# Kernel tuning notes

Hardware: AMD Instinct MI355X
Metric: run time of the kernel (lower is better)

## Reference

```python
import jax, jax.numpy as jnp
import numpy as np
import math
from jax.ops import segment_sum

TOPK_RATIO = 0.1
CLUSTER_RATIO = 0.25
K_KNN = 10


def setup_inputs() -> dict:
    key = jax.random.key(0)
    ks = jax.random.split(key, 10)
    N, C, H, W = 8, 256, 100, 352
    sc = 0.02
    return {
        "spatial_features_2d": jax.random.normal(ks[0], (N, C, H, W), jnp.float32),
        "dis_priority": jax.random.uniform(ks[1], (N, H, W), dtype=jnp.float32),
        "score_w1": jax.random.normal(ks[2], (256, 256), jnp.float32) * sc,
        "score_b1": jnp.zeros((256,), jnp.float32),
        "score_w2": jax.random.normal(ks[3], (1, 256), jnp.float32) * sc,
        "score_b2": jnp.zeros((1,), jnp.float32),
        "cls_w": jax.random.normal(ks[4], (2, 256), jnp.float32) * sc,
        "cls_b": jnp.zeros((2,), jnp.float32),
        "reg_w": jax.random.normal(ks[5], (14, 256), jnp.float32) * sc,
        "reg_b": jnp.zeros((14,), jnp.float32),
        "record_len": jnp.array([2, 3, 1, 2], jnp.int32),
    }


def _forward(x, dis_priority, score_w1, score_b1, score_w2, score_b2,
             cls_w, cls_b, reg_w, reg_b, record_len):
    N, C, H, W = x.shape
    L = H * W
    xf = x.reshape(N, C, L)  # [N,C,L]

    # --- SortSampler: per-pixel 2-layer fc score net (1x1 convs) ---
    h = jax.nn.relu(jnp.einsum('oc,ncl->nol', score_w1, xf) + score_b1[None, :, None])
    scores = jax.nn.sigmoid(jnp.einsum('oc,ncl->nol', score_w2, h) + score_b2[None, :, None])[:, 0]  # [N,L]
    weight = scores * dis_priority.reshape(N, L)
    K = max(int(math.ceil(L * TOPK_RATIO)), 1)  # static topk token count
    sort_idx = jnp.argsort(-weight, axis=1)[:, :K]              # pos_embed [N,K]
    conf = jnp.take_along_axis(weight, sort_idx, axis=1)        # [N,K]
    feats = jnp.take_along_axis(xf, sort_idx[:, None, :], axis=2)  # [N,C,K]
    src = jnp.transpose(feats, (0, 2, 1)) * conf[:, :, None]    # [N,K,C]

    # --- cluster_dpc_knn ---
    M = max(int(math.ceil(K * CLUSTER_RATIO)), 1)
    sq = jnp.sum(src * src, axis=-1)                             # [N,K]
    dist = sq[:, :, None] + sq[:, None, :] - 2.0 * jnp.einsum('nkc,njc->nkj', src, src)
    dist = jnp.maximum(dist, 0.0)                                # [N,K,K]
    dist_nearest = -jax.lax.top_k(-dist, K_KNN)[0]               # [N,K,k] smallest
    density = jnp.exp(-jnp.mean(dist_nearest, axis=-1))          # [N,K]
    density = density + jnp.arange(K, dtype=density.dtype) * 1e-6  # deterministic tie-break
    higher = density[:, None, :] > density[:, :, None]           # [N,K,K]
    dist_max = jnp.max(dist)
    d_higher = jnp.where(higher, dist, dist_max)
    delta = jnp.min(d_higher, axis=-1)                           # [N,K]
    score = delta * density
    idx_centers = jax.lax.top_k(score, M)[1]                     # [N,M]
    # assign each token to nearest cluster center
    dist_centers = jnp.take_along_axis(dist, idx_centers[:, :, None], axis=1)  # [N,M,K]
    idx_cluster = jnp.argmin(dist_centers, axis=1)               # [N,K]
    idx_cluster = idx_cluster.at[jnp.arange(N)[:, None], idx_centers].set(
        jnp.broadcast_to(jnp.arange(M), (N, M)))

    # --- merge_tokens: weighted average per cluster ---
    flat_seg = (idx_cluster + jnp.arange(N, dtype=idx_cluster.dtype)[:, None] * M).reshape(-1)
    w = conf.reshape(-1)
    all_w = segment_sum(w, flat_seg, num_segments=N * M) + 1e-6          # [N*M]
    merged = segment_sum((src * conf[:, :, None]).reshape(N * K, C), flat_seg,
                         num_segments=N * M) / all_w[:, None]
    merged = merged.reshape(N, M, C)
    # index_points: broadcast merged cluster feature back to each token
    src_tok = jnp.take_along_axis(merged, idx_cluster[:, :, None], axis=1)  # [N,K,C]
    src_ct = jnp.transpose(src_tok, (0, 2, 1))                   # [N,C,K]

    # --- scatter tokens back into BEV grid ---
    def scat(idxs, f):  # idxs [K], f [C,K]
        return jnp.zeros((C, L), f.dtype).at[:, idxs].set(f)
    bev = jax.vmap(scat)(sort_idx, src_ct)                       # [N,C,L]
    # ego CAVs (index 0 within each record) keep the full dense feature
    offsets = jnp.concatenate([jnp.zeros((1,), jnp.int32),
                               jnp.cumsum(record_len)[:-1].astype(jnp.int32)])
    is_ego = jnp.any(jnp.arange(N)[:, None] == offsets[None, :], axis=1)  # [N]
    bev = jnp.where(is_ego[:, None, None], xf, bev).reshape(N, C, H, W)

    # --- ego heads (1x1 convs) ---
    ego = x[offsets]                                              # [B,C,H,W]
    psm_ego = jnp.einsum('oc,bchw->bohw', cls_w, ego) + cls_b[None, :, None, None]
    rm_ego = jnp.einsum('oc,bchw->bohw', reg_w, ego) + reg_b[None, :, None, None]
    return bev, psm_ego, rm_ego


def reference(spatial_features_2d, dis_priority, score_w1, score_b1, score_w2, score_b2,
              cls_w, cls_b, reg_w, reg_b, record_len):
    return _forward(spatial_features_2d, dis_priority, score_w1, score_b1, score_w2,
                    score_b2, cls_w, cls_b, reg_w, reg_b, record_len)
```

## Files before the change

kernel.cpp:

```cpp
#include <hip/hip_runtime.h>
#include <hip/hip_bf16.h>

#define CCH   256
#define LPIX  35200
#define KSEL  3520
#define MCL   880
#define NBINS 16384
#define FMAXV 3.402823466e38f

__global__ void transpose_w1(const float* __restrict__ w1, float* __restrict__ w1t) {
    int o = blockIdx.x, c = threadIdx.x;
    w1t[c * 256 + o] = w1[o * 256 + c];
}

__global__ __launch_bounds__(256) void score_kernel(
    const float* __restrict__ x, const float* __restrict__ prio,
    const float* __restrict__ w1t, const float* __restrict__ b1,
    const float* __restrict__ w2, const float* __restrict__ b2,
    float* __restrict__ weight) {
    int n = blockIdx.y;
    int l0 = blockIdx.x * 64;
    int tid = threadIdx.x;
    __shared__ float W1s[16][256];
    __shared__ float Xs[16][64];
    __shared__ float spart[64][33];
    const float* xb = x + (size_t)n * CCH * LPIX;
    int to = tid >> 3;
    int tl = tid & 7;
    float acc[8][8] = {};
    for (int c0 = 0; c0 < 256; c0 += 16) {
#pragma unroll
        for (int u = 0; u < 4; u++) {
            int id = tid + u * 256;
            int cc = id >> 6, o4 = (id & 63) << 2;
            *(float4*)&W1s[cc][o4] = *(const float4*)&w1t[(size_t)(c0 + cc) * 256 + o4];
        }
        {
            int cc = tid >> 4, l4 = (tid & 15) << 2;
            *(float4*)&Xs[cc][l4] = *(const float4*)&xb[(size_t)(c0 + cc) * LPIX + l0 + l4];
        }
        __syncthreads();
#pragma unroll
        for (int cc = 0; cc < 16; cc++) {
            float a[8], bb[8];
            *(float4*)&a[0]  = *(float4*)&W1s[cc][to * 8];
            *(float4*)&a[4]  = *(float4*)&W1s[cc][to * 8 + 4];
            *(float4*)&bb[0] = *(float4*)&Xs[cc][tl * 8];
            *(float4*)&bb[4] = *(float4*)&Xs[cc][tl * 8 + 4];
#pragma unroll
            for (int i = 0; i < 8; i++)
#pragma unroll
                for (int j = 0; j < 8; j++) acc[i][j] += a[i] * bb[j];
        }
        __syncthreads();
    }
    float w2v[8], b1v[8];
    *(float4*)&b1v[0] = *(const float4*)&b1[to * 8];
    *(float4*)&b1v[4] = *(const float4*)&b1[to * 8 + 4];
    *(float4*)&w2v[0] = *(const float4*)&w2[to * 8];
    *(float4*)&w2v[4] = *(const float4*)&w2[to * 8 + 4];
#pragma unroll
    for (int j = 0; j < 8; j++) {
        float s = 0.f;
#pragma unroll
        for (int i = 0; i < 8; i++) s += w2v[i] * fmaxf(acc[i][j] + b1v[i], 0.f);
        spart[tl * 8 + j][to] = s;
    }
    __syncthreads();
    if (tid < 64) {
        float s = 0.f;
#pragma unroll
        for (int r = 0; r < 32; r++) s += spart[tid][r];
        s += b2[0];
        float sg = 1.f / (1.f + expf(-s));
        int gl = l0 + tid;
        weight[(size_t)n * LPIX + gl] = sg * prio[(size_t)n * LPIX + gl];
    }
}

__global__ void hist_kernel(const float* __restrict__ weight, int* __restrict__ hist) {
    int n = blockIdx.y;
    int i = blockIdx.x * 256 + threadIdx.x;
    if (i >= LPIX) return;
    float w = weight[(size_t)n * LPIX + i];
    int b = (int)(w * (float)NBINS);
    b = min(max(b, 0), NBINS - 1);
    atomicAdd(&hist[(size_t)n * NBINS + b], 1);
}

__global__ __launch_bounds__(256) void thr_kernel(const int* __restrict__ hist, int* __restrict__ thrbin) {
    int n = blockIdx.x, t = threadIdx.x;
    const int CH = NBINS / 256;
    __shared__ int csum[256];
    __shared__ int bfound;
    int base = NBINS - (t + 1) * CH;
    int s = 0;
    for (int i = 0; i < CH; i++) s += hist[(size_t)n * NBINS + base + i];
    csum[t] = s;
    __syncthreads();
    if (t == 0) {
        int cum = 0, sel = 255;
        for (int u = 0; u < 256; u++) {
            cum += csum[u];
            csum[u] = cum;
            if (cum >= KSEL) { sel = u; break; }
        }
        bfound = sel;
    }
    __syncthreads();
    if (t == 0) {
        int u = bfound;
        int cumBefore = (u == 0) ? 0 : csum[u - 1];
        int base2 = NBINS - (u + 1) * CH;
        int cum = cumBefore, bsel = base2;
        for (int b = base2 + CH - 1; b >= base2; b--) {
            cum += hist[(size_t)n * NBINS + b];
            if (cum >= KSEL) { bsel = b; break; }
        }
        thrbin[n] = bsel;
    }
}

__global__ void cand_kernel(const float* __restrict__ weight, const int* __restrict__ thrbin,
                            float* __restrict__ candw, int* __restrict__ cidx, int* __restrict__ ccnt) {
    int n = blockIdx.y;
    int i = blockIdx.x * 256 + threadIdx.x;
    if (i >= LPIX) return;
    float w = weight[(size_t)n * LPIX + i];
    int b = (int)(w * (float)NBINS);
    b = min(max(b, 0), NBINS - 1);
    if (b >= thrbin[n]) {
        int p = atomicAdd(&ccnt[n], 1);
        candw[(size_t)n * LPIX + p] = w;
        cidx[(size_t)n * LPIX + p] = i;
    }
}

__global__ __launch_bounds__(256) void rank_kernel(const float* __restrict__ candw, const int* __restrict__ cidx,
                                                   const int* __restrict__ ccnt,
                                                   float* __restrict__ conf, int* __restrict__ sidx) {
    int n = blockIdx.y, i = blockIdx.x;
    int cnt = ccnt[n];
    if (i >= cnt) return;
    float wi = candw[(size_t)n * LPIX + i];
    int ii = cidx[(size_t)n * LPIX + i];
    int r = 0;
    for (int j = threadIdx.x; j < cnt; j += 256) {
        float wj = candw[(size_t)n * LPIX + j];
        int ij = cidx[(size_t)n * LPIX + j];
        if (wj > wi || (wj == wi && ij < ii)) r++;
    }
    __shared__ int red[256];
    red[threadIdx.x] = r;
    __syncthreads();
    for (int s = 128; s > 0; s >>= 1) {
        if (threadIdx.x < s) red[threadIdx.x] += red[threadIdx.x + s];
        __syncthreads();
    }
    if (threadIdx.x == 0) {
        int rank = red[0];
        if (rank < KSEL) {
            sidx[(size_t)n * KSEL + rank] = ii;
            conf[(size_t)n * KSEL + rank] = wi;
        }
    }
}

__global__ __launch_bounds__(256) void gather_src(const float* __restrict__ x, const int* __restrict__ sidx,
                                                  const float* __restrict__ conf,
                                                  float* __restrict__ src, float* __restrict__ sq, int* __restrict__ inv) {
    int n = blockIdx.y, k = blockIdx.x, c = threadIdx.x;
    int idx = sidx[(size_t)n * KSEL + k];
    float cf = conf[(size_t)n * KSEL + k];
    float v = x[((size_t)n * CCH + c) * LPIX + idx] * cf;
    src[((size_t)n * KSEL + k) * CCH + c] = v;
    __shared__ float red[256];
    red[c] = v * v;
    __syncthreads();
    for (int s = 128; s > 0; s >>= 1) {
        if (c < s) red[c] += red[c + s];
        __syncthreads();
    }
    if (c == 0) {
        sq[(size_t)n * KSEL + k] = red[0];
        inv[(size_t)n * LPIX + idx] = k;
    }
}

__global__ __launch_bounds__(256) void dist_gemm(const float* __restrict__ src, const float* __restrict__ sq,
                                                 float* __restrict__ dist, int n0) {
    int n = n0 + blockIdx.z;
    const float* S = src + (size_t)n * KSEL * CCH;
    const float* sqn = sq + (size_t)n * KSEL;
    float* D = dist + (size_t)blockIdx.z * KSEL * KSEL;
    int b = blockIdx.x;
    int iT = (int)((sqrtf(8.f * (float)b + 1.f) - 1.f) * 0.5f);
    while ((iT + 1) * (iT + 2) / 2 <= b) iT++;
    while (iT * (iT + 1) / 2 > b) iT--;
    int jT = b - iT * (iT + 1) / 2;
    int bi = iT * 128, bj = jT * 128;
    __shared__ float As[16][128], Bs[16][128];
    int tid = threadIdx.x;
    int ti = tid >> 4, to = tid & 15;
    int sr = tid >> 1;
    int sc = (tid & 1) * 8;
    int ra = min(bi + sr, KSEL - 1);
    int rb = min(bj + sr, KSEL - 1);
    float acc[8][8] = {};
    for (int c0 = 0; c0 < CCH; c0 += 16) {
        float4 a0 = *(const float4*)&S[(size_t)ra * CCH + c0 + sc];
        float4 a1 = *(const float4*)&S[(size_t)ra * CCH + c0 + sc + 4];
        float4 b0 = *(const float4*)&S[(size_t)rb * CCH + c0 + sc];
        float4 b1 = *(const float4*)&S[(size_t)rb * CCH + c0 + sc + 4];
        __syncthreads();
        As[sc + 0][sr] = a0.x; As[sc + 1][sr] = a0.y; As[sc + 2][sr] = a0.z; As[sc + 3][sr] = a0.w;
        As[sc + 4][sr] = a1.x; As[sc + 5][sr] = a1.y; As[sc + 6][sr] = a1.z; As[sc + 7][sr] = a1.w;
        Bs[sc + 0][sr] = b0.x; Bs[sc + 1][sr] = b0.y; Bs[sc + 2][sr] = b0.z; Bs[sc + 3][sr] = b0.w;
        Bs[sc + 4][sr] = b1.x; Bs[sc + 5][sr] = b1.y; Bs[sc + 6][sr] = b1.z; Bs[sc + 7][sr] = b1.w;
        __syncthreads();
#pragma unroll
        for (int cc = 0; cc < 16; cc++) {
            float a[8], bb[8];
            *(float4*)&a[0]  = *(float4*)&As[cc][ti * 8];
            *(float4*)&a[4]  = *(float4*)&As[cc][ti * 8 + 4];
            *(float4*)&bb[0] = *(float4*)&Bs[cc][to * 8];
            *(float4*)&bb[4] = *(float4*)&Bs[cc][to * 8 + 4];
#pragma unroll
            for (int i = 0; i < 8; i++)
#pragma unroll
                for (int j = 0; j < 8; j++) acc[i][j] += a[i] * bb[j];
        }
    }
    if (bi + ti * 8 < KSEL && bj + to * 8 < KSEL) {
        float sqj[8];
        *(float4*)&sqj[0] = *(const float4*)&sqn[bj + to * 8];
        *(float4*)&sqj[4] = *(const float4*)&sqn[bj + to * 8 + 4];
        float d[8][8];
#pragma unroll
        for (int i = 0; i < 8; i++) {
            float si = sqn[bi + ti * 8 + i];
#pragma unroll
            for (int j = 0; j < 8; j++) d[i][j] = fmaxf(si + sqj[j] - 2.f * acc[i][j], 0.f);
        }
#pragma unroll
        for (int i = 0; i < 8; i++) {
            int gi = bi + ti * 8 + i;
            *(float4*)&D[(size_t)gi * KSEL + bj + to * 8]     = *(float4*)&d[i][0];
            *(float4*)&D[(size_t)gi * KSEL + bj + to * 8 + 4] = *(float4*)&d[i][4];
        }
        if (iT != jT) {
#pragma unroll
            for (int j = 0; j < 8; j++) {
                int gj = bj + to * 8 + j;
                float4 t0, t1;
                t0.x = d[0][j]; t0.y = d[1][j]; t0.z = d[2][j]; t0.w = d[3][j];
                t1.x = d[4][j]; t1.y = d[5][j]; t1.z = d[6][j]; t1.w = d[7][j];
                *(float4*)&D[(size_t)gj * KSEL + bi + ti * 8]     = t0;
                *(float4*)&D[(size_t)gj * KSEL + bi + ti * 8 + 4] = t1;
            }
        }
    }
}

__global__ __launch_bounds__(256) void knn_density(const float* __restrict__ dist, float* __restrict__ density, int n0) {
    int n = n0 + blockIdx.y;
    int row = threadIdx.x >> 6;
    int lane = threadIdx.x & 63;
    int i = blockIdx.x * 4 + row;
    const float4* row4 = (const float4*)(dist + (size_t)blockIdx.y * KSEL * KSEL + (size_t)i * KSEL);
    float tt[10];
#pragma unroll
    for (int r = 0; r < 10; r++) tt[r] = FMAXV;
    for (int j4 = lane; j4 < KSEL / 4; j4 += 64) {
        float4 v4 = row4[j4];
        float vv[4] = {v4.x, v4.y, v4.z, v4.w};
#pragma unroll
        for (int q = 0; q < 4; q++) {
            float v = vv[q];
            if (v < tt[9]) {
                tt[9] = v;
#pragma unroll
                for (int r = 9; r > 0; r--) {
                    if (tt[r] < tt[r - 1]) { float tmp = tt[r - 1]; tt[r - 1] = tt[r]; tt[r] = tmp; }
                }
            }
        }
    }
    __shared__ float ls[4][64][10];
#pragma unroll
    for (int r = 0; r < 10; r++) ls[row][lane][r] = tt[r];
    __syncthreads();
    for (int s = 32; s >= 1; s >>= 1) {
        if (lane < s) {
            float out[10];
            int ia = 0, ib = 0;
#pragma unroll
            for (int r = 0; r < 10; r++) {
                float va = ls[row][lane][ia], vb = ls[row][lane + s][ib];
                if (va <= vb) { out[r] = va; ia++; } else { out[r] = vb; ib++; }
            }
#pragma unroll
            for (int r = 0; r < 10; r++) ls[row][lane][r] = out[r];
        }
        __syncthreads();
    }
    if (lane == 0) {
        float sum = 0.f;
#pragma unroll
        for (int r = 0; r < 10; r++) sum += ls[row][0][r];
        density[(size_t)n * KSEL + i] = expf(-sum * 0.1f) + (float)i * 1e-6f;
    }
}

__global__ __launch_bounds__(256) void delta_score(const float* __restrict__ dist, const float* __restrict__ density,
                                                   float* __restrict__ scoreb, int n0) {
    int n = n0 + blockIdx.y;
    int i = blockIdx.x;
    const float4* row = (const float4*)(dist + (size_t)blockIdx.y * KSEL * KSEL + (size_t)i * KSEL);
    const float* dn = density + (size_t)n * KSEL;
    const float4* dn4 = (const float4*)dn;
    float di = dn[i];
    float mn = FMAXV;
    for (int j4 = threadIdx.x; j4 < KSEL / 4; j4 += 256) {
        float4 d = dn4[j4];
        float4 v = row[j4];
        if (d.x > di) mn = fminf(mn, v.x);
        if (d.y > di) mn = fminf(mn, v.y);
        if (d.z > di) mn = fminf(mn, v.z);
        if (d.w > di) mn = fminf(mn, v.w);
    }
    __shared__ float red[256];
    red[threadIdx.x] = mn;
    __syncthreads();
    for (int s = 128; s > 0; s >>= 1) {
        if (threadIdx.x < s) red[threadIdx.x] = fminf(red[threadIdx.x], red[threadIdx.x + s]);
        __syncthreads();
    }
    if (threadIdx.x == 0) {
        float d = red[0];
        scoreb[(size_t)n * KSEL + i] = (d == FMAXV) ? FMAXV : d * di;
    }
}

__global__ __launch_bounds__(256) void center_rank(const float* __restrict__ scoreb, int* __restrict__ centers,
                                                   int* __restrict__ crank, int n0) {
    int n = n0 + blockIdx.y;
    int i = blockIdx.x;
    const float* sc = scoreb + (size_t)n * KSEL;
    float si = sc[i];
    int r = 0;
    for (int j = threadIdx.x; j < KSEL; j += 256) {
        float sj = sc[j];
        if (sj > si || (sj == si && j < i)) r++;
    }
    __shared__ int red[256];
    red[threadIdx.x] = r;
    __syncthreads();
    for (int s = 128; s > 0; s >>= 1) {
        if (threadIdx.x < s) red[threadIdx.x] += red[threadIdx.x + s];
        __syncthreads();
    }
    if (threadIdx.x == 0) {
        int rank = red[0];
        if (rank < MCL) {
            centers[(size_t)n * MCL + rank] = i;
            crank[(size_t)n * KSEL + i] = rank;
        }
    }
}

__global__ __launch_bounds__(256) void assign_kernel(const float* __restrict__ dist, const int* __restrict__ centers,
                                                     const int* __restrict__ crank, int* __restrict__ clus, int n0) {
    int n = n0 + blockIdx.y;
    const float* D = dist + (size_t)blockIdx.y * KSEL * KSEL;
    int kl = threadIdx.x & 63, mc = threadIdx.x >> 6;
    int k = blockIdx.x * 64 + kl;
    const int* ctr = centers + (size_t)n * MCL;
    float mn = FMAXV;
    int am = MCL;
    for (int m = mc * 220; m < (mc + 1) * 220; m++) {
        float v = D[(size_t)ctr[m] * KSEL + k];
        if (v < mn) { mn = v; am = m; }
    }
    __shared__ float mv[4][64];
    __shared__ int mi[4][64];
    mv[mc][kl] = mn;
    mi[mc][kl] = am;
    __syncthreads();
    if (mc == 0) {
        float best = mv[0][kl];
        int bm = mi[0][kl];
#pragma unroll
        for (int c = 1; c < 4; c++) {
            float v = mv[c][kl];
            int im = mi[c][kl];
            if (v < best || (v == best && im < bm)) { best = v; bm = im; }
        }
        int cr = crank[(size_t)n * KSEL + k];
        clus[(size_t)n * KSEL + k] = (cr >= 0) ? cr : bm;
    }
}

__global__ void merge_w(const float* __restrict__ conf, const int* __restrict__ clus, float* __restrict__ allw, int n0) {
    int n = n0 + blockIdx.y;
    int k = blockIdx.x * 256 + threadIdx.x;
    if (k >= KSEL) return;
    atomicAdd(&allw[(size_t)n * MCL + clus[(size_t)n * KSEL + k]], conf[(size_t)n * KSEL + k]);
}

__global__ void merge_feat(const float* __restrict__ src, const float* __restrict__ conf,
                           const int* __restrict__ clus, float* __restrict__ merged, int n0) {
    int n = n0 + blockIdx.y;
    int k = blockIdx.x, c = threadIdx.x;
    float v = src[((size_t)n * KSEL + k) * CCH + c] * conf[(size_t)n * KSEL + k];
    atomicAdd(&merged[((size_t)n * MCL + clus[(size_t)n * KSEL + k]) * CCH + c], v);
}

__global__ void merged_div(float* __restrict__ merged, const float* __restrict__ allw) {
    int nm = blockIdx.x, c = threadIdx.x;
    merged[(size_t)nm * CCH + c] /= (allw[nm] + 1e-6f);
}

__global__ __launch_bounds__(256) void bev_kernel(const float* __restrict__ x, const int* __restrict__ inv,
                                                  const int* __restrict__ clus, const float* __restrict__ merged,
                                                  const int* __restrict__ reclen, int B, float* __restrict__ out) {
    int n = blockIdx.y;
    int l0 = (blockIdx.x * 256 + threadIdx.x) * 4;
    if (l0 >= LPIX) return;
    bool ego = false;
    {
        int off = 0;
        for (int b = 0; b < B; b++) {
            if (n == off) { ego = true; break; }
            off += reclen[b];
        }
    }
    size_t base = (size_t)n * CCH * LPIX + l0;
    if (ego) {
        for (int c = 0; c < CCH; c++)
            *(float4*)&out[base + (size_t)c * LPIX] = *(const float4*)&x[base + (size_t)c * LPIX];
    } else {
        const float* mr0; const float* mr1; const float* mr2; const float* mr3;
        {
            int t0 = inv[(size_t)n * LPIX + l0 + 0];
            int t1 = inv[(size_t)n * LPIX + l0 + 1];
            int t2 = inv[(size_t)n * LPIX + l0 + 2];
            int t3 = inv[(size_t)n * LPIX + l0 + 3];
            mr0 = (t0 >= 0) ? merged + ((size_t)n * MCL + clus[(size_t)n * KSEL + t0]) * CCH : nullptr;
            mr1 = (t1 >= 0) ? merged + ((size_t)n * MCL + clus[(size_t)n * KSEL + t1]) * CCH : nullptr;
            mr2 = (t2 >= 0) ? merged + ((size_t)n * MCL + clus[(size_t)n * KSEL + t2]) * CCH : nullptr;
            mr3 = (t3 >= 0) ? merged + ((size_t)n * MCL + clus[(size_t)n * KSEL + t3]) * CCH : nullptr;
        }
        for (int c = 0; c < CCH; c++) {
            float4 v;
            v.x = mr0 ? mr0[c] : 0.f;
            v.y = mr1 ? mr1[c] : 0.f;
            v.z = mr2 ? mr2[c] : 0.f;
            v.w = mr3 ? mr3[c] : 0.f;
            *(float4*)&out[base + (size_t)c * LPIX] = v;
        }
    }
}

__global__ __launch_bounds__(256) void heads_kernel(const float* __restrict__ x,
                                                    const float* __restrict__ clsw, const float* __restrict__ clsb,
                                                    const float* __restrict__ regw, const float* __restrict__ regb,
                                                    const int* __restrict__ reclen,
                                                    float* __restrict__ psm, float* __restrict__ rm) {
    int b = blockIdx.y;
    int l0 = (blockIdx.x * 256 + threadIdx.x) * 4;
    __shared__ float ws[16][256];
    __shared__ float bs[16];
    for (int i = threadIdx.x; i < 16 * 256; i += 256) {
        int o = i >> 8, c = i & 255;
        ws[o][c] = (o < 2) ? clsw[o * 256 + c] : regw[(o - 2) * 256 + c];
    }
    if (threadIdx.x < 16) bs[threadIdx.x] = (threadIdx.x < 2) ? clsb[threadIdx.x] : regb[threadIdx.x - 2];
    __syncthreads();
    if (l0 >= LPIX) return;
    int off = 0;
    for (int u = 0; u < b; u++) off += reclen[u];
    const float* xb = x + (size_t)off * CCH * LPIX;
    float acc[16][4] = {};
    for (int c = 0; c < CCH; c++) {
        float4 v = *(const float4*)&xb[(size_t)c * LPIX + l0];
#pragma unroll
        for (int o = 0; o < 16; o++) {
            float w = ws[o][c];
            acc[o][0] += w * v.x; acc[o][1] += w * v.y; acc[o][2] += w * v.z; acc[o][3] += w * v.w;
        }
    }
#pragma unroll
    for (int o = 0; o < 2; o++) {
        float4 r;
        r.x = acc[o][0] + bs[o]; r.y = acc[o][1] + bs[o]; r.z = acc[o][2] + bs[o]; r.w = acc[o][3] + bs[o];
        *(float4*)&psm[((size_t)b * 2 + o) * LPIX + l0] = r;
    }
#pragma unroll
    for (int o = 0; o < 14; o++) {
        float4 r;
        float bb = bs[o + 2];
        r.x = acc[o + 2][0] + bb; r.y = acc[o + 2][1] + bb; r.z = acc[o + 2][2] + bb; r.w = acc[o + 2][3] + bb;
        *(float4*)&rm[((size_t)b * 14 + o) * LPIX + l0] = r;
    }
}

extern "C" void kernel_launch(void* const* d_in, const int* in_sizes, int n_in,
                              void* d_out, int out_size, void* d_ws, size_t ws_size,
                              hipStream_t stream) {
    const float* x    = (const float*)d_in[0];
    const float* prio = (const float*)d_in[1];
    const float* w1   = (const float*)d_in[2];
    const float* b1   = (const float*)d_in[3];
    const float* w2   = (const float*)d_in[4];
    const float* b2   = (const float*)d_in[5];
    const float* clsw = (const float*)d_in[6];
    const float* clsb = (const float*)d_in[7];
    const float* regw = (const float*)d_in[8];
    const float* regb = (const float*)d_in[9];
    const int* reclen = (const int*)d_in[10];
    int N = in_sizes[0] / (CCH * LPIX);
    int B = in_sizes[10];
    float* out = (float*)d_out;

    char* p = (char*)d_ws;
    size_t off = 0;
    auto alloc = [&](size_t bytes) -> void* {
        void* r = p + off;
        off += (bytes + 255) & ~(size_t)255;
        return r;
    };
    float* w1t     = (float*)alloc(256 * 256 * 4);
    float* weight  = (float*)alloc((size_t)N * LPIX * 4);
    int*   hist    = (int*)alloc((size_t)N * NBINS * 4);
    int*   thrbin  = (int*)alloc((size_t)N * 4);
    int*   ccnt    = (int*)alloc((size_t)N * 4);
    float* candw   = (float*)alloc((size_t)N * LPIX * 4);
    int*   cidx    = (int*)alloc((size_t)N * LPIX * 4);
    int*   sidx    = (int*)alloc((size_t)N * KSEL * 4);
    float* conf    = (float*)alloc((size_t)N * KSEL * 4);
    float* src     = (float*)alloc((size_t)N * KSEL * CCH * 4);
    float* sq      = (float*)alloc((size_t)N * KSEL * 4);
    int*   inv     = (int*)alloc((size_t)N * LPIX * 4);
    float* density = (float*)alloc((size_t)N * KSEL * 4);
    float* scoreb  = (float*)alloc((size_t)N * KSEL * 4);
    int*   centers = (int*)alloc((size_t)N * MCL * 4);
    int*   crank   = (int*)alloc((size_t)N * KSEL * 4);
    int*   clus    = (int*)alloc((size_t)N * KSEL * 4);
    float* allw    = (float*)alloc((size_t)N * MCL * 4);
    float* merged  = (float*)alloc((size_t)N * MCL * CCH * 4);
    const size_t distB = (size_t)KSEL * KSEL * 4;
    size_t rem = (ws_size > off) ? (ws_size - off) : 0;
    int nd = (int)(rem / distB);
    if (nd < 1) nd = 1;
    if (nd > N) nd = N;
    float* dist = (float*)alloc(distB * nd);

    hipMemsetAsync(hist, 0, (size_t)N * NBINS * 4, stream);
    hipMemsetAsync(ccnt, 0, (size_t)N * 4, stream);
    hipMemsetAsync(inv, 0xFF, (size_t)N * LPIX * 4, stream);
    hipMemsetAsync(crank, 0xFF, (size_t)N * KSEL * 4, stream);
    hipMemsetAsync(allw, 0, (size_t)N * MCL * 4, stream);
    hipMemsetAsync(merged, 0, (size_t)N * MCL * CCH * 4, stream);

    transpose_w1<<<256, 256, 0, stream>>>(w1, w1t);
    score_kernel<<<dim3(LPIX / 64, N), 256, 0, stream>>>(x, prio, w1t, b1, w2, b2, weight);
    hist_kernel<<<dim3((LPIX + 255) / 256, N), 256, 0, stream>>>(weight, hist);
    thr_kernel<<<N, 256, 0, stream>>>(hist, thrbin);
    cand_kernel<<<dim3((LPIX + 255) / 256, N), 256, 0, stream>>>(weight, thrbin, candw, cidx, ccnt);
    rank_kernel<<<dim3(8192, N), 256, 0, stream>>>(candw, cidx, ccnt, conf, sidx);
    gather_src<<<dim3(KSEL, N), 256, 0, stream>>>(x, sidx, conf, src, sq, inv);

    const int TI = (KSEL + 127) / 128;
    const int NT = TI * (TI + 1) / 2;
    for (int g = 0; g < N; g += nd) {
        int nb = (N - g < nd) ? (N - g) : nd;
        dist_gemm<<<dim3(NT, 1, nb), 256, 0, stream>>>(src, sq, dist, g);
        knn_density<<<dim3(KSEL / 4, nb), 256, 0, stream>>>(dist, density, g);
        delta_score<<<dim3(KSEL, nb), 256, 0, stream>>>(dist, density, scoreb, g);
        center_rank<<<dim3(KSEL, nb), 256, 0, stream>>>(scoreb, centers, crank, g);
        assign_kernel<<<dim3(KSEL / 64, nb), 256, 0, stream>>>(dist, centers, crank, clus, g);
        merge_w<<<dim3((KSEL + 255) / 256, nb), 256, 0, stream>>>(conf, clus, allw, g);
        merge_feat<<<dim3(KSEL, nb), 256, 0, stream>>>(src, conf, clus, merged, g);
    }
    merged_div<<<N * MCL, 256, 0, stream>>>(merged, allw);
    bev_kernel<<<dim3((LPIX / 4 + 255) / 256, N), 256, 0, stream>>>(x, inv, clus, merged, reclen, B, out);

    float* psm = out + (size_t)N * CCH * LPIX;
    float* rm  = psm + (size_t)B * 2 * LPIX;
    heads_kernel<<<dim3((LPIX / 4 + 255) / 256, B), 256, 0, stream>>>(x, clsw, clsb, regw, regb, reclen, psm, rm);
}
```

Baseline: 1.575 ms.

## Use split-bf16 MFMA for score net and pairwise distance GEMMs

Replaces the FP32 scalar-FMA GEMMs in the score network and the pairwise distance computation with MFMA bf16 matrix instructions. Each operand is split three ways (hi/mid/lo bf16), and six cross-product MFMAs per tile recover near-FP32 accuracy. The distance kernel drops the triangular-tile scheme with mirrored writes and computes the full square grid directly. This trades 6x more matrix ops, extra split storage and bandwidth, and the lost symmetry savings for much higher MFMA throughput.

```diff
diff --git a/kernel.cpp b/kernel.cpp
--- a/kernel.cpp
+++ b/kernel.cpp
@@ -8,73 +8,111 @@
 #define NBINS 16384
 #define FMAXV 3.402823466e38f
 
-__global__ void transpose_w1(const float* __restrict__ w1, float* __restrict__ w1t) {
-    int o = blockIdx.x, c = threadIdx.x;
-    w1t[c * 256 + o] = w1[o * 256 + c];
-}
-
-__global__ __launch_bounds__(256) void score_kernel(
+typedef __bf16 bf16x8 __attribute__((ext_vector_type(8)));
+typedef float  f32x4  __attribute__((ext_vector_type(4)));
+typedef unsigned short ushort_t;
+
+__device__ __forceinline__ void split3(float v, __bf16* h, __bf16* m, __bf16* l) {
+    __bf16 a = (__bf16)v;
+    float r = v - (float)a;
+    __bf16 b = (__bf16)r;
+    float r2 = r - (float)b;
+    *h = a; *m = b; *l = (__bf16)r2;
+}
+
+#define MFMA6(ACC, AH, AM, AL, BH, BM, BL)                                   \
+    ACC = __builtin_amdgcn_mfma_f32_16x16x32_bf16(AH, BH, ACC, 0, 0, 0);     \
+    ACC = __builtin_amdgcn_mfma_f32_16x16x32_bf16(AH, BM, ACC, 0, 0, 0);     \
+    ACC = __builtin_amdgcn_mfma_f32_16x16x32_bf16(AM, BH, ACC, 0, 0, 0);     \
+    ACC = __builtin_amdgcn_mfma_f32_16x16x32_bf16(AH, BL, ACC, 0, 0, 0);     \
+    ACC = __builtin_amdgcn_mfma_f32_16x16x32_bf16(AM, BM, ACC, 0, 0, 0);     \
+    ACC = __builtin_amdgcn_mfma_f32_16x16x32_bf16(AL, BH, ACC, 0, 0, 0);
+
+__global__ void split_w1(const float* __restrict__ w1, __bf16* __restrict__ h,
+                         __bf16* __restrict__ m, __bf16* __restrict__ l) {
+    int i = blockIdx.x * 256 + threadIdx.x;
+    split3(w1[i], &h[i], &m[i], &l[i]);
+}
+
+__global__ __launch_bounds__(256) void score_mfma(
     const float* __restrict__ x, const float* __restrict__ prio,
-    const float* __restrict__ w1t, const float* __restrict__ b1,
-    const float* __restrict__ w2, const float* __restrict__ b2,
+    const __bf16* __restrict__ w1h, const __bf16* __restrict__ w1m, const __bf16* __restrict__ w1l,
+    const float* __restrict__ b1, const float* __restrict__ w2, const float* __restrict__ b2,
     float* __restrict__ weight) {
     int n = blockIdx.y;
     int l0 = blockIdx.x * 64;
-    int tid = threadIdx.x;
-    __shared__ float W1s[16][256];
-    __shared__ float Xs[16][64];
-    __shared__ float spart[64][33];
+    int tid = threadIdx.x, w = tid >> 6, lane = tid & 63;
+    int lrow = lane & 15, kg = lane >> 4;
+    __shared__ __align__(16) __bf16 Xs[3][64][40];
+    __shared__ float spart[64][17];
     const float* xb = x + (size_t)n * CCH * LPIX;
-    int to = tid >> 3;
-    int tl = tid & 7;
-    float acc[8][8] = {};
-    for (int c0 = 0; c0 < 256; c0 += 16) {
-#pragma unroll
-        for (int u = 0; u < 4; u++) {
-            int id = tid + u * 256;
-            int cc = id >> 6, o4 = (id & 63) << 2;
-            *(float4*)&W1s[cc][o4] = *(const float4*)&w1t[(size_t)(c0 + cc) * 256 + o4];
-        }
-        {
-            int cc = tid >> 4, l4 = (tid & 15) << 2;
-            *(float4*)&Xs[cc][l4] = *(const float4*)&xb[(size_t)(c0 + cc) * LPIX + l0 + l4];
-        }
-        __syncthreads();
-#pragma unroll
-        for (int cc = 0; cc < 16; cc++) {
-            float a[8], bb[8];
-            *(float4*)&a[0]  = *(float4*)&W1s[cc][to * 8];
-            *(float4*)&a[4]  = *(float4*)&W1s[cc][to * 8 + 4];
-            *(float4*)&bb[0] = *(float4*)&Xs[cc][tl * 8];
-            *(float4*)&bb[4] = *(float4*)&Xs[cc][tl * 8 + 4];
-#pragma unroll
-            for (int i = 0; i < 8; i++)
-#pragma unroll
-                for (int j = 0; j < 8; j++) acc[i][j] += a[i] * bb[j];
-        }
-        __syncthreads();
-    }
-    float w2v[8], b1v[8];
-    *(float4*)&b1v[0] = *(const float4*)&b1[to * 8];
-    *(float4*)&b1v[4] = *(const float4*)&b1[to * 8 + 4];
-    *(float4*)&w2v[0] = *(const float4*)&w2[to * 8];
-    *(float4*)&w2v[4] = *(const float4*)&w2[to * 8 + 4];
-#pragma unroll
-    for (int j = 0; j < 8; j++) {
-        float s = 0.f;
-#pragma unroll
-        for (int i = 0; i < 8; i++) s += w2v[i] * fmaxf(acc[i][j] + b1v[i], 0.f);
-        spart[tl * 8 + j][to] = s;
-    }
+    f32x4 acc[4][4];
+#pragma unroll
+    for (int i = 0; i < 4; i++)
+#pragma unroll
+        for (int j = 0; j < 4; j++) acc[i][j] = (f32x4){0.f, 0.f, 0.f, 0.f};
+
+    int cp = tid >> 4, lg = tid & 15;
+    for (int c0 = 0; c0 < 256; c0 += 32) {
+        __syncthreads();
+        float4 f0 = *(const float4*)&xb[(size_t)(c0 + 2 * cp) * LPIX + l0 + lg * 4];
+        float4 f1 = *(const float4*)&xb[(size_t)(c0 + 2 * cp + 1) * LPIX + l0 + lg * 4];
+        float p0[4] = {f0.x, f0.y, f0.z, f0.w};
+        float p1[4] = {f1.x, f1.y, f1.z, f1.w};
+#pragma unroll
+        for (int q = 0; q < 4; q++) {
+            __bf16 h0, m0, lo0, h1, m1, lo1;
+            split3(p0[q], &h0, &m0, &lo0);
+            split3(p1[q], &h1, &m1, &lo1);
+            int l = lg * 4 + q;
+            *(unsigned*)&Xs[0][l][2 * cp] = ((unsigned)*(ushort_t*)&h1 << 16) | *(ushort_t*)&h0;
+            *(unsigned*)&Xs[1][l][2 * cp] = ((unsigned)*(ushort_t*)&m1 << 16) | *(ushort_t*)&m0;
+            *(unsigned*)&Xs[2][l][2 * cp] = ((unsigned)*(ushort_t*)&lo1 << 16) | *(ushort_t*)&lo0;
+        }
+        __syncthreads();
+        bf16x8 bfh[4], bfm[4], bfl[4];
+#pragma unroll
+        for (int fj = 0; fj < 4; fj++) {
+            bfh[fj] = *(const bf16x8*)&Xs[0][fj * 16 + lrow][kg * 8];
+            bfm[fj] = *(const bf16x8*)&Xs[1][fj * 16 + lrow][kg * 8];
+            bfl[fj] = *(const bf16x8*)&Xs[2][fj * 16 + lrow][kg * 8];
+        }
+#pragma unroll
+        for (int fi = 0; fi < 4; fi++) {
+            size_t ao = (size_t)(w * 64 + fi * 16 + lrow) * 256 + c0 + kg * 8;
+            bf16x8 ah = *(const bf16x8*)&w1h[ao];
+            bf16x8 am = *(const bf16x8*)&w1m[ao];
+            bf16x8 al = *(const bf16x8*)&w1l[ao];
+#pragma unroll
+            for (int fj = 0; fj < 4; fj++) {
+                MFMA6(acc[fi][fj], ah, am, al, bfh[fj], bfm[fj], bfl[fj]);
+            }
+        }
+    }
+    float ps[4] = {0.f, 0.f, 0.f, 0.f};
+#pragma unroll
+    for (int fi = 0; fi < 4; fi++) {
+        int ob = w * 64 + fi * 16 + kg * 4;
+        float4 b1v = *(const float4*)&b1[ob];
+        float4 w2v = *(const float4*)&w2[ob];
+        float b1a[4] = {b1v.x, b1v.y, b1v.z, b1v.w};
+        float w2a[4] = {w2v.x, w2v.y, w2v.z, w2v.w};
+#pragma unroll
+        for (int r = 0; r < 4; r++)
+#pragma unroll
+            for (int fj = 0; fj < 4; fj++)
+                ps[fj] += w2a[r] * fmaxf(acc[fi][fj][r] + b1a[r], 0.f);
+    }
+#pragma unroll
+    for (int fj = 0; fj < 4; fj++) spart[fj * 16 + lrow][w * 4 + kg] = ps[fj];
     __syncthreads();
     if (tid < 64) {
         float s = 0.f;
 #pragma unroll
-        for (int r = 0; r < 32; r++) s += spart[tid][r];
+        for (int r = 0; r < 16; r++) s += spart[tid][r];
         s += b2[0];
         float sg = 1.f / (1.f + expf(-s));
-        int gl = l0 + tid;
-        weight[(size_t)n * LPIX + gl] = sg * prio[(size_t)n * LPIX + gl];
+        weight[(size_t)n * LPIX + l0 + tid] = sg * prio[(size_t)n * LPIX + l0 + tid];
     }
 }
 
@@ -168,12 +206,19 @@
 
 __global__ __launch_bounds__(256) void gather_src(const float* __restrict__ x, const int* __restrict__ sidx,
                                                   const float* __restrict__ conf,
-                                                  float* __restrict__ src, float* __restrict__ sq, int* __restrict__ inv) {
+                                                  float* __restrict__ src,
+                                                  __bf16* __restrict__ sh, __bf16* __restrict__ sm,
+                                                  __bf16* __restrict__ sl,
+                                                  float* __restrict__ sq, int* __restrict__ inv) {
     int n = blockIdx.y, k = blockIdx.x, c = threadIdx.x;
     int idx = sidx[(size_t)n * KSEL + k];
     float cf = conf[(size_t)n * KSEL + k];
     float v = x[((size_t)n * CCH + c) * LPIX + idx] * cf;
-    src[((size_t)n * KSEL + k) * CCH + c] = v;
+    size_t o = ((size_t)n * KSEL + k) * CCH + c;
+    src[o] = v;
+    __bf16 h, m, l;
+    split3(v, &h, &m, &l);
+    sh[o] = h; sm[o] = m; sl[o] = l;
     __shared__ float red[256];
     red[c] = v * v;
     __syncthreads();
@@ -187,76 +232,73 @@
     }
 }
 
-__global__ __launch_bounds__(256) void dist_gemm(const float* __restrict__ src, const float* __restrict__ sq,
-                                                 float* __restrict__ dist, int n0) {
+__global__ __launch_bounds__(256) void dist_mfma(
+    const __bf16* __restrict__ sh, const __bf16* __restrict__ sm, const __bf16* __restrict__ sl,
+    const float* __restrict__ sq, float* __restrict__ dist, int n0) {
     int n = n0 + blockIdx.z;
-    const float* S = src + (size_t)n * KSEL * CCH;
+    const size_t nb = (size_t)n * KSEL * CCH;
     const float* sqn = sq + (size_t)n * KSEL;
     float* D = dist + (size_t)blockIdx.z * KSEL * KSEL;
-    int b = blockIdx.x;
-    int iT = (int)((sqrtf(8.f * (float)b + 1.f) - 1.f) * 0.5f);
-    while ((iT + 1) * (iT + 2) / 2 <= b) iT++;
-    while (iT * (iT + 1) / 2 > b) iT--;
-    int jT = b - iT * (iT + 1) / 2;
-    int bi = iT * 128, bj = jT * 128;
-    __shared__ float As[16][128], Bs[16][128];
-    int tid = threadIdx.x;
-    int ti = tid >> 4, to = tid & 15;
-    int sr = tid >> 1;
-    int sc = (tid & 1) * 8;
-    int ra = min(bi + sr, KSEL - 1);
-    int rb = min(bj + sr, KSEL - 1);
-    float acc[8][8] = {};
-    for (int c0 = 0; c0 < CCH; c0 += 16) {
-        float4 a0 = *(const float4*)&S[(size_t)ra * CCH + c0 + sc];
-        float4 a1 = *(const float4*)&S[(size_t)ra * CCH + c0 + sc + 4];
-        float4 b0 = *(const float4*)&S[(size_t)rb * CCH + c0 + sc];
-        float4 b1 = *(const float4*)&S[(size_t)rb * CCH + c0 + sc + 4];
-        __syncthreads();
-        As[sc + 0][sr] = a0.x; As[sc + 1][sr] = a0.y; As[sc + 2][sr] = a0.z; As[sc + 3][sr] = a0.w;
-        As[sc + 4][sr] = a1.x; As[sc + 5][sr] = a1.y; As[sc + 6][sr] = a1.z; As[sc + 7][sr] = a1.w;
-        Bs[sc + 0][sr] = b0.x; Bs[sc + 1][sr] = b0.y; Bs[sc + 2][sr] = b0.z; Bs[sc + 3][sr] = b0.w;
-        Bs[sc + 4][sr] = b1.x; Bs[sc + 5][sr] = b1.y; Bs[sc + 6][sr] = b1.z; Bs[sc + 7][sr] = b1.w;
-        __syncthreads();
-#pragma unroll
-        for (int cc = 0; cc < 16; cc++) {
-            float a[8], bb[8];
-            *(float4*)&a[0]  = *(float4*)&As[cc][ti * 8];
-            *(float4*)&a[4]  = *(float4*)&As[cc][ti * 8 + 4];
-            *(float4*)&bb[0] = *(float4*)&Bs[cc][to * 8];
-            *(float4*)&bb[4] = *(float4*)&Bs[cc][to * 8 + 4];
-#pragma unroll
-            for (int i = 0; i < 8; i++)
-#pragma unroll
-                for (int j = 0; j < 8; j++) acc[i][j] += a[i] * bb[j];
-        }
-    }
-    if (bi + ti * 8 < KSEL && bj + to * 8 < KSEL) {
-        float sqj[8];
-        *(float4*)&sqj[0] = *(const float4*)&sqn[bj + to * 8];
-        *(float4*)&sqj[4] = *(const float4*)&sqn[bj + to * 8 + 4];
-        float d[8][8];
-#pragma unroll
-        for (int i = 0; i < 8; i++) {
-            float si = sqn[bi + ti * 8 + i];
-#pragma unroll
-            for (int j = 0; j < 8; j++) d[i][j] = fmaxf(si + sqj[j] - 2.f * acc[i][j], 0.f);
-        }
-#pragma unroll
-        for (int i = 0; i < 8; i++) {
-            int gi = bi + ti * 8 + i;
-            *(float4*)&D[(size_t)gi * KSEL + bj + to * 8]     = *(float4*)&d[i][0];
-            *(float4*)&D[(size_t)gi * KSEL + bj + to * 8 + 4] = *(float4*)&d[i][4];
-        }
-        if (iT != jT) {
-#pragma unroll
-            for (int j = 0; j < 8; j++) {
-                int gj = bj + to * 8 + j;
-                float4 t0, t1;
-                t0.x = d[0][j]; t0.y = d[1][j]; t0.z = d[2][j]; t0.w = d[3][j];
-                t1.x = d[4][j]; t1.y = d[5][j]; t1.z = d[6][j]; t1.w = d[7][j];
-                *(float4*)&D[(size_t)gj * KSEL + bi + ti * 8]     = t0;
-                *(float4*)&D[(size_t)gj * KSEL + bi + ti * 8 + 4] = t1;
+    int bi = blockIdx.y * 128, bj = blockIdx.x * 128;
+    __shared__ __align__(16) __bf16 As[3][128][40], Bs[3][128][40];
+    int tid = threadIdx.x, w = tid >> 6, lane = tid & 63;
+    int lrow = lane & 15, kg = lane >> 4;
+    int wr = w >> 1, wc = w & 1;
+    f32x4 acc[4][4];
+#pragma unroll
+    for (int i = 0; i < 4; i++)
+#pragma unroll
+        for (int j = 0; j < 4; j++) acc[i][j] = (f32x4){0.f, 0.f, 0.f, 0.f};
+
+    int sr = tid & 127, g2 = tid >> 7;
+    size_t ra = nb + (size_t)min(bi + sr, KSEL - 1) * CCH;
+    size_t rb = nb + (size_t)min(bj + sr, KSEL - 1) * CCH;
+    for (int c0 = 0; c0 < 256; c0 += 32) {
+        __syncthreads();
+#pragma unroll
+        for (int hh = 0; hh < 2; hh++) {
+            int cg = hh * 2 + g2;
+            *(bf16x8*)&As[0][sr][cg * 8] = *(const bf16x8*)&sh[ra + c0 + cg * 8];
+            *(bf16x8*)&As[1][sr][cg * 8] = *(const bf16x8*)&sm[ra + c0 + cg * 8];
+            *(bf16x8*)&As[2][sr][cg * 8] = *(const bf16x8*)&sl[ra + c0 + cg * 8];
+            *(bf16x8*)&Bs[0][sr][cg * 8] = *(const bf16x8*)&sh[rb + c0 + cg * 8];
+            *(bf16x8*)&Bs[1][sr][cg * 8] = *(const bf16x8*)&sm[rb + c0 + cg * 8];
+            *(bf16x8*)&Bs[2][sr][cg * 8] = *(const bf16x8*)&sl[rb + c0 + cg * 8];
+        }
+        __syncthreads();
+        bf16x8 bfh[4], bfm[4], bfl[4];
+#pragma unroll
+        for (int fj = 0; fj < 4; fj++) {
+            bfh[fj] = *(const bf16x8*)&Bs[0][wc * 64 + fj * 16 + lrow][kg * 8];
+            bfm[fj] = *(const bf16x8*)&Bs[1][wc * 64 + fj * 16 + lrow][kg * 8];
+            bfl[fj] = *(const bf16x8*)&Bs[2][wc * 64 + fj * 16 + lrow][kg * 8];
+        }
+#pragma unroll
+        for (int fi = 0; fi < 4; fi++) {
+            int arow = wr * 64 + fi * 16 + lrow;
+            bf16x8 ah = *(const bf16x8*)&As[0][arow][kg * 8];
+            bf16x8 am = *(const bf16x8*)&As[1][arow][kg * 8];
+            bf16x8 al = *(const bf16x8*)&As[2][arow][kg * 8];
+#pragma unroll
+            for (int fj = 0; fj < 4; fj++) {
+                MFMA6(acc[fi][fj], ah, am, al, bfh[fj], bfm[fj], bfl[fj]);
+            }
+        }
+    }
+#pragma unroll
+    for (int fi = 0; fi < 4; fi++) {
+        int gi0 = bi + wr * 64 + fi * 16;
+        if (gi0 >= KSEL) continue;
+#pragma unroll
+        for (int fj = 0; fj < 4; fj++) {
+            int gj0 = bj + wc * 64 + fj * 16;
+            if (gj0 >= KSEL) continue;
+            int gj = gj0 + lrow;
+            float sj = sqn[gj];
+#pragma unroll
+            for (int r = 0; r < 4; r++) {
+                int gi = gi0 + kg * 4 + r;
+                D[(size_t)gi * KSEL + gj] = fmaxf(sqn[gi] + sj - 2.f * acc[fi][fj][r], 0.f);
             }
         }
     }
@@ -530,7 +572,9 @@
         off += (bytes + 255) & ~(size_t)255;
         return r;
     };
-    float* w1t     = (float*)alloc(256 * 256 * 4);
+    __bf16* w1h    = (__bf16*)alloc(256 * 256 * 2);
+    __bf16* w1m    = (__bf16*)alloc(256 * 256 * 2);
+    __bf16* w1l    = (__bf16*)alloc(256 * 256 * 2);
     float* weight  = (float*)alloc((size_t)N * LPIX * 4);
     int*   hist    = (int*)alloc((size_t)N * NBINS * 4);
     int*   thrbin  = (int*)alloc((size_t)N * 4);
@@ -540,6 +584,9 @@
     int*   sidx    = (int*)alloc((size_t)N * KSEL * 4);
     float* conf    = (float*)alloc((size_t)N * KSEL * 4);
     float* src     = (float*)alloc((size_t)N * KSEL * CCH * 4);
+    __bf16* srch   = (__bf16*)alloc((size_t)N * KSEL * CCH * 2);
+    __bf16* srcm   = (__bf16*)alloc((size_t)N * KSEL * CCH * 2);
+    __bf16* srcl   = (__bf16*)alloc((size_t)N * KSEL * CCH * 2);
     float* sq      = (float*)alloc((size_t)N * KSEL * 4);
     int*   inv     = (int*)alloc((size_t)N * LPIX * 4);
     float* density = (float*)alloc((size_t)N * KSEL * 4);
@@ -563,19 +610,18 @@
     hipMemsetAsync(allw, 0, (size_t)N * MCL * 4, stream);
     hipMemsetAsync(merged, 0, (size_t)N * MCL * CCH * 4, stream);
 
-    transpose_w1<<<256, 256, 0, stream>>>(w1, w1t);
-    score_kernel<<<dim3(LPIX / 64, N), 256, 0, stream>>>(x, prio, w1t, b1, w2, b2, weight);
+    split_w1<<<256, 256, 0, stream>>>(w1, w1h, w1m, w1l);
+    score_mfma<<<dim3(LPIX / 64, N), 256, 0, stream>>>(x, prio, w1h, w1m, w1l, b1, w2, b2, weight);
     hist_kernel<<<dim3((LPIX + 255) / 256, N), 256, 0, stream>>>(weight, hist);
     thr_kernel<<<N, 256, 0, stream>>>(hist, thrbin);
     cand_kernel<<<dim3((LPIX + 255) / 256, N), 256, 0, stream>>>(weight, thrbin, candw, cidx, ccnt);
     rank_kernel<<<dim3(8192, N), 256, 0, stream>>>(candw, cidx, ccnt, conf, sidx);
-    gather_src<<<dim3(KSEL, N), 256, 0, stream>>>(x, sidx, conf, src, sq, inv);
+    gather_src<<<dim3(KSEL, N), 256, 0, stream>>>(x, sidx, conf, src, srch, srcm, srcl, sq, inv);
 
     const int TI = (KSEL + 127) / 128;
-    const int NT = TI * (TI + 1) / 2;
     for (int g = 0; g < N; g += nd) {
         int nb = (N - g < nd) ? (N - g) : nd;
-        dist_gemm<<<dim3(NT, 1, nb), 256, 0, stream>>>(src, sq, dist, g);
+        dist_mfma<<<dim3(TI, TI, nb), 256, 0, stream>>>(srch, srcm, srcl, sq, dist, g);
         knn_density<<<dim3(KSEL / 4, nb), 256, 0, stream>>>(dist, density, g);
         delta_score<<<dim3(KSEL, nb), 256, 0, stream>>>(dist, density, scoreb, g);
         center_rank<<<dim3(KSEL, nb), 256, 0, stream>>>(scoreb, centers, crank, g);
```

After: 1.650 ms. +4.8%, slower.
